# Kernel optimization log

Measured on AMD Instinct MI355X. Metric: run time of the kernel, lower is better.

## Reference

```python
import jax, jax.numpy as jnp
import numpy as np

B, T, D = 4, 2048, 1024
H = 16
DK = D // H


def setup_inputs() -> dict:
    key = jax.random.key(0)
    k1, k2, k3, k4 = jax.random.split(key, 4)
    x = jax.random.normal(k1, (B, T, D), dtype=jnp.float32)
    prefix_lengths = jax.random.randint(k2, (B,), 0, 1024, dtype=jnp.int64)
    # torch Linear weights: [out_features, in_features], scaled like kaiming-uniform-ish
    W_qkv = jax.random.normal(k3, (3 * D, D), dtype=jnp.float32) / np.sqrt(D)
    W_o = jax.random.normal(k4, (D, D), dtype=jnp.float32) / np.sqrt(D)
    return {"x": x, "prefix_lengths": prefix_lengths, "W_qkv": W_qkv, "W_o": W_o}


def _prefix_lm_mask(seq_len, prefix_lengths):
    # True where attention is BLOCKED.
    pos = jnp.arange(seq_len)
    key_pos = pos[None, None, :]          # [1,1,T]
    query_pos = pos[None, :, None]        # [1,T,1]
    prefix = prefix_lengths[:, None, None]  # [B,1,1]
    q_in_pre = query_pos < prefix
    k_in_pre = key_pos < prefix
    block_pre_to_suf = q_in_pre & ~k_in_pre
    block_future_suf = ~q_in_pre & ~k_in_pre & (key_pos > query_pos)
    return block_pre_to_suf | block_future_suf  # [B,T,T]


def reference(x, prefix_lengths, W_qkv, W_o):
    Bb, Tt, Cc = x.shape
    qkv = x @ W_qkv.T                     # [B,T,3D]
    qkv = qkv.reshape(Bb, Tt, 3, H, DK).transpose(2, 0, 3, 1, 4)  # [3,B,H,T,dk]
    q, k, v = qkv[0], qkv[1], qkv[2]
    scale = 1.0 / np.sqrt(DK).astype(np.float32)
    attn = jnp.einsum('bhqd,bhkd->bhqk', q, k) * scale  # [B,H,T,T]
    pl = jnp.clip(prefix_lengths.astype(jnp.int32), 0, Tt)
    mask = _prefix_lm_mask(Tt, pl)        # [B,T,T]
    attn = jnp.where(mask[:, None, :, :], -jnp.inf, attn)
    attn = jax.nn.softmax(attn, axis=-1)
    out = jnp.einsum('bhqk,bhkd->bhqd', attn, v)  # [B,H,T,dk]
    out = out.transpose(0, 2, 1, 3).reshape(Bb, Tt, Cc)
    return out @ W_o.T
```

## Files before the change

### kernel.cpp

```cpp
#include <hip/hip_runtime.h>
#include <stdint.h>

#define NB 4
#define NT 2048
#define ND 1024
#define NH 16
#define NDK 64
#define NTD 3072

typedef __attribute__((ext_vector_type(8))) short short8;
typedef __attribute__((ext_vector_type(4))) float f32x4;
typedef unsigned short u16;
typedef unsigned int u32;

__device__ __forceinline__ u16 f2bf(float f) {
    u32 u = __builtin_bit_cast(u32, f);
    u += 0x7fffu + ((u >> 16) & 1u);
    return (u16)(u >> 16);
}
__device__ __forceinline__ float bf2f(u16 s) {
    u32 u = ((u32)s) << 16;
    return __builtin_bit_cast(float, u);
}

__device__ __forceinline__ void gl_lds16(const u16* g, u16* l) {
    __builtin_amdgcn_global_load_lds(
        (const __attribute__((address_space(1))) u32*)g,
        (__attribute__((address_space(3))) u32*)l, 16, 0, 0);
}

__device__ __forceinline__ int swz(int row, int col) {
    return row * 32 + ((((col >> 3) ^ (row >> 1) ^ (row >> 3)) & 3) << 3) + (col & 7);
}

__global__ __launch_bounds__(256) void cvt_all(const float* __restrict__ x,
                                               const float* __restrict__ wqkv,
                                               const float* __restrict__ wo,
                                               u16* __restrict__ xb,
                                               u16* __restrict__ wqb,
                                               u16* __restrict__ wob) {
    const int n0 = NB * NT * ND;
    const int n1 = 3 * ND * ND;
    int i = (blockIdx.x * 256 + threadIdx.x) * 8;
    const float* src;
    u16* dst;
    if (i < n0) {
        src = x + i; dst = xb + i;
    } else if (i < n0 + n1) {
        src = wqkv + (i - n0); dst = wqb + (i - n0);
    } else {
        src = wo + (i - n0 - n1); dst = wob + (i - n0 - n1);
    }
    float4 a = *(const float4*)(src);
    float4 b = *(const float4*)(src + 4);
    short8 r;
    r[0] = (short)f2bf(a.x); r[1] = (short)f2bf(a.y);
    r[2] = (short)f2bf(a.z); r[3] = (short)f2bf(a.w);
    r[4] = (short)f2bf(b.x); r[5] = (short)f2bf(b.y);
    r[6] = (short)f2bf(b.z); r[7] = (short)f2bf(b.w);
    *(short8*)(dst) = r;
}

template <typename OutT>
__global__ __launch_bounds__(256) void gemm_bt(const u16* __restrict__ A,
                                               const u16* __restrict__ Bm,
                                               OutT* __restrict__ C,
                                               int M, int N, int K) {
    __shared__ __align__(16) u16 As[128 * 32];
    __shared__ __align__(16) u16 Bs[128 * 32];
    const int tid  = threadIdx.x;
    const int wave = tid >> 6, lane = tid & 63;
    const int quad = lane >> 4, l16 = lane & 15;
    const int wm = wave >> 1, wn = wave & 1;
    const int fid = blockIdx.y * gridDim.x + blockIdx.x;
    const int bx = ((fid & 7) << 3) | ((fid >> 3) & 7);
    const int by = fid >> 6;
    const int row0 = bx * 128, col0 = by * 128;

    f32x4 acc[4][4];
#pragma unroll
    for (int i = 0; i < 4; ++i)
#pragma unroll
        for (int j = 0; j < 4; ++j) acc[i][j] = (f32x4){0.f, 0.f, 0.f, 0.f};

    const u16* Ag = A + (size_t)(row0 + (tid >> 2)) * K + ((tid & 3) * 8);
    const u16* Bg = Bm + (size_t)(col0 + (tid >> 2)) * K + ((tid & 3) * 8);
    const size_t stride64 = (size_t)64 * K;
    u16* As0 = As + wave * 512;
    u16* As1 = As + 2048 + wave * 512;
    u16* Bs0 = Bs + wave * 512;
    u16* Bs1 = Bs + 2048 + wave * 512;

    for (int k0 = 0; k0 < K; k0 += 32) {
        gl_lds16(Ag + k0, As0);
        gl_lds16(Ag + k0 + stride64, As1);
        gl_lds16(Bg + k0, Bs0);
        gl_lds16(Bg + k0 + stride64, Bs1);
        __syncthreads();
        short8 af[4], bfr[4];
#pragma unroll
        for (int mi = 0; mi < 4; ++mi)
            af[mi] = *(const short8*)&As[(wm * 64 + mi * 16 + l16) * 32 + quad * 8];
#pragma unroll
        for (int ni = 0; ni < 4; ++ni)
            bfr[ni] = *(const short8*)&Bs[(wn * 64 + ni * 16 + l16) * 32 + quad * 8];
#pragma unroll
        for (int mi = 0; mi < 4; ++mi)
#pragma unroll
            for (int ni = 0; ni < 4; ++ni)
                acc[mi][ni] = __builtin_amdgcn_mfma_f32_16x16x32_bf16(
                    af[mi], bfr[ni], acc[mi][ni], 0, 0, 0);
        __syncthreads();
    }

#pragma unroll
    for (int mi = 0; mi < 4; ++mi) {
#pragma unroll
        for (int ni = 0; ni < 4; ++ni) {
            const int r = row0 + wm * 64 + mi * 16 + quad * 4;
            const int c = col0 + wn * 64 + ni * 16 + l16;
#pragma unroll
            for (int rr = 0; rr < 4; ++rr) {
                float v = acc[mi][ni][rr];
                if constexpr (sizeof(OutT) == 2)
                    C[(size_t)(r + rr) * N + c] = (OutT)f2bf(v);
                else
                    C[(size_t)(r + rr) * N + c] = (OutT)v;
            }
        }
    }
}

__global__ __launch_bounds__(512, 2) void gemm_qk256(const u16* __restrict__ A,
                                                     const u16* __restrict__ Bm,
                                                     u16* __restrict__ Cq) {
    __shared__ __align__(16) u16 rbA[2][8192];
    __shared__ __align__(16) u16 rbB[2][8192];
    u16* const rbAf = &rbA[0][0];
    u16* const rbBf = &rbB[0][0];
    const int tid  = threadIdx.x;
    const int wave = tid >> 6, lane = tid & 63;
    const int quad = lane >> 4, l16 = lane & 15;
    const int wm = wave >> 2, wn = wave & 3;
    const int K = ND;
    const int fid = blockIdx.x;
    const int bx = (fid & 7) * 4 + (fid >> 6);
    const int by = (fid >> 3) & 7;
    const int row0 = bx * 256, col0 = by * 256;

    const int sr0 = tid >> 3, sl0 = (tid & 7) ^ (sr0 & 7);
    const int a1 = 512 + tid;
    const int sr1 = a1 >> 3, sl1 = (a1 & 7) ^ (sr1 & 7);
    const int r0i = 2 * sr0 + (sl0 >> 2), k0i = (sl0 & 3) * 8;
    const int r1i = 2 * sr1 + (sl1 >> 2), k1i = (sl1 & 3) * 8;
    const u16* srcA0 = A + (size_t)(row0 + r0i) * K + k0i;
    const u16* srcA1 = A + (size_t)(row0 + r1i) * K + k1i;
    const u16* srcB0 = Bm + (size_t)(col0 + r0i) * K + k0i;
    const u16* srcB1 = Bm + (size_t)(col0 + r1i) * K + k1i;
    const int ldsc0 = wave * 512;
    const int ldsc1 = 4096 + wave * 512;

    int aoff[8], boff[4];
#pragma unroll
    for (int mi = 0; mi < 8; ++mi) {
        const int row = wm * 128 + mi * 16 + l16;
        const int srow = row >> 1;
        const int slot = ((((row & 1) << 2) | quad) ^ (srow & 7));
        aoff[mi] = srow * 64 + slot * 8;
    }
#pragma unroll
    for (int ni = 0; ni < 4; ++ni) {
        const int row = wn * 64 + ni * 16 + l16;
        const int srow = row >> 1;
        const int slot = ((((row & 1) << 2) | quad) ^ (srow & 7));
        boff[ni] = srow * 64 + slot * 8;
    }

    f32x4 acc[8][4];
#pragma unroll
    for (int i = 0; i < 8; ++i)
#pragma unroll
        for (int j = 0; j < 4; ++j) acc[i][j] = (f32x4){0.f, 0.f, 0.f, 0.f};

    gl_lds16(srcA0, rbAf + ldsc0);
    gl_lds16(srcA1, rbAf + ldsc1);
    gl_lds16(srcB0, rbBf + ldsc0);
    gl_lds16(srcB1, rbBf + ldsc1);
    __syncthreads();

#define QK_TILE(T, TB, NB_)                                                    \
    {                                                                          \
        if ((T) + 1 < 32) {                                                    \
            const int ko = ((T) + 1) * 32;                                     \
            gl_lds16(srcA0 + ko, rbAf + (NB_) + ldsc0);                        \
            gl_lds16(srcA1 + ko, rbAf + (NB_) + ldsc1);                        \
            gl_lds16(srcB0 + ko, rbBf + (NB_) + ldsc0);                        \
            gl_lds16(srcB1 + ko, rbBf + (NB_) + ldsc1);                        \
        }                                                                      \
        short8 af[4], bfr[4];                                                  \
        _Pragma("unroll") for (int mi = 0; mi < 4; ++mi)                       \
            af[mi] = *(const short8*)&rbAf[(TB) + aoff[mi]];                   \
        _Pragma("unroll") for (int ni = 0; ni < 4; ++ni)                       \
            bfr[ni] = *(const short8*)&rbBf[(TB) + boff[ni]];                  \
        __builtin_amdgcn_s_setprio(1);                                         \
        _Pragma("unroll") for (int mi = 0; mi < 4; ++mi)                       \
            _Pragma("unroll") for (int ni = 0; ni < 4; ++ni)                   \
                acc[mi][ni] = __builtin_amdgcn_mfma_f32_16x16x32_bf16(         \
                    af[mi], bfr[ni], acc[mi][ni], 0, 0, 0);                    \
        __builtin_amdgcn_s_setprio(0);                                         \
        __builtin_amdgcn_s_barrier();                                          \
        short8 af2[4];                                                         \
        _Pragma("unroll") for (int mi = 0; mi < 4; ++mi)                       \
            af2[mi] = *(const short8*)&rbAf[(TB) + aoff[4 + mi]];              \
        __builtin_amdgcn_s_setprio(1);                                         \
        _Pragma("unroll") for (int mi = 0; mi < 4; ++mi)                       \
            _Pragma("unroll") for (int ni = 0; ni < 4; ++ni)                   \
                acc[4 + mi][ni] = __builtin_amdgcn_mfma_f32_16x16x32_bf16(     \
                    af2[mi], bfr[ni], acc[4 + mi][ni], 0, 0, 0);               \
        __builtin_amdgcn_s_setprio(0);                                         \
        __syncthreads();                                                       \
    }

    for (int t2 = 0; t2 < 32; t2 += 2) {
        QK_TILE(t2, 0, 8192);
        QK_TILE(t2 + 1, 8192, 0);
    }
#undef QK_TILE

#pragma unroll
    for (int mi = 0; mi < 8; ++mi) {
#pragma unroll
        for (int ni = 0; ni < 4; ++ni) {
            const int r = row0 + wm * 128 + mi * 16 + quad * 4;
            const int c = col0 + wn * 64 + ni * 16 + l16;
#pragma unroll
            for (int rr = 0; rr < 4; ++rr)
                Cq[(size_t)(r + rr) * NTD + c] = f2bf(acc[mi][ni][rr]);
        }
    }
}

__global__ __launch_bounds__(256) void gemm_v(const u16* __restrict__ A,
                                              const u16* __restrict__ Bm,
                                              u16* __restrict__ vtb) {
    const int Kd = ND;
    __shared__ __align__(16) u16 As[128 * 32];
    __shared__ __align__(16) u16 Bs[128 * 32];
    const int tid  = threadIdx.x;
    const int wave = tid >> 6, lane = tid & 63;
    const int quad = lane >> 4, l16 = lane & 15;
    const int wm = wave >> 1, wn = wave & 1;
    const int fid = blockIdx.y * gridDim.x + blockIdx.x;
    const int bx = ((fid & 7) << 3) | ((fid >> 3) & 7);
    const int by = fid >> 6;
    const int row0 = bx * 128, col0 = 2048 + by * 128;

    f32x4 acc[4][4];
#pragma unroll
    for (int i = 0; i < 4; ++i)
#pragma unroll
        for (int j = 0; j < 4; ++j) acc[i][j] = (f32x4){0.f, 0.f, 0.f, 0.f};

    const u16* Ag = A + (size_t)(row0 + (tid >> 2)) * Kd + ((tid & 3) * 8);
    const u16* Bg = Bm + (size_t)(col0 + (tid >> 2)) * Kd + ((tid & 3) * 8);
    const size_t stride64 = (size_t)64 * Kd;
    u16* As0 = As + wave * 512;
    u16* As1 = As + 2048 + wave * 512;
    u16* Bs0 = Bs + wave * 512;
    u16* Bs1 = Bs + 2048 + wave * 512;

    for (int k0 = 0; k0 < Kd; k0 += 32) {
        gl_lds16(Ag + k0, As0);
        gl_lds16(Ag + k0 + stride64, As1);
        gl_lds16(Bg + k0, Bs0);
        gl_lds16(Bg + k0 + stride64, Bs1);
        __syncthreads();
        short8 af[4], bfr[4];
#pragma unroll
        for (int mi = 0; mi < 4; ++mi)
            af[mi] = *(const short8*)&As[(wm * 64 + mi * 16 + l16) * 32 + quad * 8];
#pragma unroll
        for (int ni = 0; ni < 4; ++ni)
            bfr[ni] = *(const short8*)&Bs[(wn * 64 + ni * 16 + l16) * 32 + quad * 8];
#pragma unroll
        for (int mi = 0; mi < 4; ++mi)
#pragma unroll
            for (int ni = 0; ni < 4; ++ni)
                acc[mi][ni] = __builtin_amdgcn_mfma_f32_16x16x32_bf16(
                    af[mi], bfr[ni], acc[mi][ni], 0, 0, 0);
        __syncthreads();
    }

    const int hb = ((col0 - 2048) >> 6) + wn;
    const int bq = (row0 + wm * 64) >> 11;
    const int tb = (row0 + wm * 64) & 2047;
    u16* Ovt = vtb + (size_t)(bq * NH + hb) * 64 * NT + tb;
#pragma unroll
    for (int phase = 0; phase < 2; ++phase) {
        __syncthreads();
        if ((wave >> 1) == phase) {
            u16* L = (wave & 1) ? Bs : As;
#pragma unroll
            for (int mi = 0; mi < 4; ++mi) {
                const int r4 = mi * 4 + quad;
#pragma unroll
                for (int ni = 0; ni < 4; ++ni) {
                    const int cl = ni * 16 + l16;
                    u32 lo = (u32)f2bf(acc[mi][ni][0]) | ((u32)f2bf(acc[mi][ni][1]) << 16);
                    u32 hi = (u32)f2bf(acc[mi][ni][2]) | ((u32)f2bf(acc[mi][ni][3]) << 16);
                    u32* p = (u32*)&L[cl * 64 + (((r4 ^ cl) & 15) << 2)];
                    p[0] = lo; p[1] = hi;
                }
            }
#pragma unroll
            for (int rep = 0; rep < 8; ++rep) {
                const int cl = (lane >> 3) + rep * 8;
                const int tc = lane & 7;
                const u32* p0 = (const u32*)&L[cl * 64 + ((((2 * tc) ^ cl) & 15) << 2)];
                const u32* p1 = (const u32*)&L[cl * 64 + ((((2 * tc + 1) ^ cl) & 15) << 2)];
                u32 o0 = p0[0], o1 = p0[1], o2 = p1[0], o3 = p1[1];
                u32* q = (u32*)(Ovt + (size_t)cl * NT + tc * 8);
                q[0] = o0; q[1] = o1; q[2] = o2; q[3] = o3;
            }
        }
    }
}

#define GETREG_XCC_ID 6164
__global__ __launch_bounds__(256) void flash_prefix(const u16* __restrict__ qkv,
                                                    const u16* __restrict__ vt,
                                                    const int* __restrict__ plen,
                                                    u16* __restrict__ attn,
                                                    u32* __restrict__ ctr) {
    __shared__ __align__(16) u16 Vt2[2][2048];
    __shared__ __align__(16) u16 Kt2[2][2048];
    __shared__ __align__(16) u16 Pl[4 * 512];
    __shared__ int taskS;

    const int tid  = threadIdx.x;
    const int wave = tid >> 6, lane = tid & 63;
    const int quad = lane >> 4, l16 = lane & 15;
    const float QSCALE = 0.18033688f;
    const int ldsoff = wave * 512;

    short8 ones;
#pragma unroll
    for (int j = 0; j < 8; ++j) ones[j] = (short)0x3F80;

    const bool is64 = (plen[1] == 0) && (plen[3] == 0);
    const int xcd = (int)(__builtin_amdgcn_s_getreg(GETREG_XCC_ID) & 7);
    int q = xcd;

    for (;;) {
        if (tid == 0) taskS = (int)atomicAdd(ctr + q * 16, 1u);
        __syncthreads();
        const int pos = taskS;
        if (pos >= 256) {
            q = (q + 1) & 7;
            if (q == xcd) break;
            continue;
        }

        const int bh = (q << 3) | (pos & 7);
        const int b = bh >> 4, h = bh & 15;
        const int q0 = (31 - (pos >> 3)) * 64;

        int P = is64 ? plen[2 * b] : plen[b];
        P = P < 0 ? 0 : (P > NT ? NT : P);

        const u16* Qg = qkv + (size_t)b * NT * NTD + h * NDK;
        const u16* Kg = Qg + ND;
        const u16* Vtb = vt + (size_t)bh * 64 * NT;
        const int qbase = q0 + wave * 16;
        u16* Pw = Pl + wave * 512;

        const int vrow = tid >> 2;
        const int vtq = (tid ^ (vrow >> 1) ^ (vrow >> 3)) & 3;
        const u16* vsrc = Vtb + (size_t)vrow * NT + vtq * 8;
        const int krow = tid >> 3;
        const int kc = (tid ^ krow) & 7;
        const u16* ksrc = Kg + (size_t)krow * NTD + kc * 8;

        short8 qa[2];
#pragma unroll
        for (int kd = 0; kd < 2; ++kd) {
            short8 tq = *(const short8*)(Qg + (size_t)(qbase + l16) * NTD + kd * 32 + quad * 8);
#pragma unroll
            for (int j = 0; j < 8; ++j)
                tq[j] = (short)f2bf(bf2f((u16)tq[j]) * QSCALE);
            qa[kd] = tq;
        }

        f32x4 o[4];
#pragma unroll
        for (int nt = 0; nt < 4; ++nt) o[nt] = (f32x4){0.f, 0.f, 0.f, 0.f};
        f32x4 lsum = (f32x4){0.f, 0.f, 0.f, 0.f};

        int kl[4];
#pragma unroll
        for (int rr = 0; rr < 4; ++rr) {
            const int qrow = qbase + quad * 4 + rr;
            kl[rr] = (qrow < P) ? P : (qrow + 1);
        }
        const int klmin = (qbase < P) ? P : (qbase + 1);
        const int kmax = (q0 + 64 > P) ? (q0 + 64) : P;

        gl_lds16(vsrc, &Vt2[0][ldsoff]);
        gl_lds16(ksrc, &Kt2[0][ldsoff]);
        int buf = 0;

        for (int k0 = 0; k0 < kmax; k0 += 32) {
            __syncthreads();
            if (k0 + 32 < kmax) {
                gl_lds16(vsrc + (k0 + 32), &Vt2[buf ^ 1][ldsoff]);
                gl_lds16(ksrc + (size_t)(k0 + 32) * NTD, &Kt2[buf ^ 1][ldsoff]);
            }
            const u16* Kb = Kt2[buf];
            const u16* Vb = Vt2[buf];

            f32x4 s[2];
#pragma unroll
            for (int ni = 0; ni < 2; ++ni) {
                s[ni] = (f32x4){0.f, 0.f, 0.f, 0.f};
#pragma unroll
                for (int kd = 0; kd < 2; ++kd) {
                    const int r = ni * 16 + l16;
                    const short8 kb = *(const short8*)&Kb[r * 64 + ((((kd * 4 + quad) ^ r) & 7) << 3)];
                    s[ni] = __builtin_amdgcn_mfma_f32_16x16x32_bf16(qa[kd], kb, s[ni], 0, 0, 0);
                }
            }

            const bool full = (k0 + 32 <= klmin);
#pragma unroll
            for (int ni = 0; ni < 2; ++ni) {
#pragma unroll
                for (int rr = 0; rr < 4; ++rr) {
                    float sv = s[ni][rr];
                    if (!full) {
                        const int kpos = k0 + ni * 16 + l16;
                        sv = (kpos < kl[rr]) ? sv : -1e30f;
                    }
                    const float p = exp2f(sv);
                    const u32 u = __builtin_bit_cast(u32, p) + 0x8000u;
                    Pw[swz(quad * 4 + rr, ni * 16 + l16)] = (u16)(u >> 16);
                }
            }

            const short8 pa = *(const short8*)&Pw[swz(l16, quad * 8)];
            lsum = __builtin_amdgcn_mfma_f32_16x16x32_bf16(pa, ones, lsum, 0, 0, 0);
#pragma unroll
            for (int nt = 0; nt < 4; ++nt) {
                const short8 vb = *(const short8*)&Vb[swz(nt * 16 + l16, quad * 8)];
                o[nt] = __builtin_amdgcn_mfma_f32_16x16x32_bf16(pa, vb, o[nt], 0, 0, 0);
            }
            buf ^= 1;
        }

#pragma unroll
        for (int rr = 0; rr < 4; ++rr) {
            const float inv = 1.0f / lsum[rr];
            const size_t rowoff = (size_t)(b * NT + qbase + quad * 4 + rr) * ND + h * NDK;
#pragma unroll
            for (int nt = 0; nt < 4; ++nt)
                attn[rowoff + nt * 16 + l16] = f2bf(o[nt][rr] * inv);
        }
    }
}

extern "C" void kernel_launch(void* const* d_in, const int* in_sizes, int n_in,
                              void* d_out, int out_size, void* d_ws, size_t ws_size,
                              hipStream_t stream) {
    const float* x    = (const float*)d_in[0];
    const int*   plen = (const int*)d_in[1];
    const float* wqkv = (const float*)d_in[2];
    const float* wo   = (const float*)d_in[3];
    float* out = (float*)d_out;

    char* ws = (char*)d_ws;
    u16* xb   = (u16*)(ws);
    u16* wqb  = (u16*)(ws + 16777216);
    u16* wob  = (u16*)(ws + 23068672);
    u16* qkv  = (u16*)(ws + 25165824);
    u16* attn = (u16*)(ws + 75497472);
    u16* vtb  = (u16*)(ws + 92274688);
    u32* ctr  = (u32*)(ws + 75496960);

    hipMemsetAsync(ctr, 0, 512, stream);

    cvt_all<<<6144, 256, 0, stream>>>(x, wqkv, wo, xb, wqb, wob);

    gemm_qk256<<<256, 512, 0, stream>>>(xb, wqb, qkv);

    gemm_v<<<dim3(64, 8), 256, 0, stream>>>(xb, wqb, vtb);

    flash_prefix<<<1024, 256, 0, stream>>>(qkv, vtb, plen, attn, ctr);

    gemm_bt<float><<<dim3(64, 8), 256, 0, stream>>>(attn, wob, out, NB * NT, ND, ND);
}
```

Measured before the change: 292.1 us.

## Deepen QK GEMM LDS pipeline to four stages with vmcnt-based waits

Replaces the double-buffered LDS ring in the QK projection GEMM with a four-buffer ring that keeps three K-tiles of global-to-LDS loads in flight. Explicit s_waitcnt vmcnt counts replace the per-tile __syncthreads, leaving one barrier per iteration, and the mid-tile barrier is dropped. This is meant to hide global load latency and cut synchronisation. In exchange LDS use doubles to 128KB per block, which may limit the two-blocks-per-CU occupancy requested by the launch bounds.

```diff
diff --git a/kernel.cpp b/kernel.cpp
--- a/kernel.cpp
+++ b/kernel.cpp
@@ -134,10 +134,8 @@
 __global__ __launch_bounds__(512, 2) void gemm_qk256(const u16* __restrict__ A,
                                                      const u16* __restrict__ Bm,
                                                      u16* __restrict__ Cq) {
-    __shared__ __align__(16) u16 rbA[2][8192];
-    __shared__ __align__(16) u16 rbB[2][8192];
-    u16* const rbAf = &rbA[0][0];
-    u16* const rbBf = &rbB[0][0];
+    __shared__ __align__(16) u16 rbA[4][8192];
+    __shared__ __align__(16) u16 rbB[4][8192];
     const int tid  = threadIdx.x;
     const int wave = tid >> 6, lane = tid & 63;
     const int quad = lane >> 4, l16 = lane & 15;
@@ -182,50 +180,60 @@
 #pragma unroll
         for (int j = 0; j < 4; ++j) acc[i][j] = (f32x4){0.f, 0.f, 0.f, 0.f};
 
-    gl_lds16(srcA0, rbAf + ldsc0);
-    gl_lds16(srcA1, rbAf + ldsc1);
-    gl_lds16(srcB0, rbBf + ldsc0);
-    gl_lds16(srcB1, rbBf + ldsc1);
-    __syncthreads();
-
-#define QK_TILE(T, TB, NB_)                                                    \
+#define QK_STAGE(T)                                                            \
     {                                                                          \
-        if ((T) + 1 < 32) {                                                    \
-            const int ko = ((T) + 1) * 32;                                     \
-            gl_lds16(srcA0 + ko, rbAf + (NB_) + ldsc0);                        \
-            gl_lds16(srcA1 + ko, rbAf + (NB_) + ldsc1);                        \
-            gl_lds16(srcB0 + ko, rbBf + (NB_) + ldsc0);                        \
-            gl_lds16(srcB1 + ko, rbBf + (NB_) + ldsc1);                        \
-        }                                                                      \
-        short8 af[4], bfr[4];                                                  \
-        _Pragma("unroll") for (int mi = 0; mi < 4; ++mi)                       \
-            af[mi] = *(const short8*)&rbAf[(TB) + aoff[mi]];                   \
-        _Pragma("unroll") for (int ni = 0; ni < 4; ++ni)                       \
-            bfr[ni] = *(const short8*)&rbBf[(TB) + boff[ni]];                  \
-        __builtin_amdgcn_s_setprio(1);                                         \
-        _Pragma("unroll") for (int mi = 0; mi < 4; ++mi)                       \
-            _Pragma("unroll") for (int ni = 0; ni < 4; ++ni)                   \
-                acc[mi][ni] = __builtin_amdgcn_mfma_f32_16x16x32_bf16(         \
-                    af[mi], bfr[ni], acc[mi][ni], 0, 0, 0);                    \
-        __builtin_amdgcn_s_setprio(0);                                         \
-        __builtin_amdgcn_s_barrier();                                          \
-        short8 af2[4];                                                         \
-        _Pragma("unroll") for (int mi = 0; mi < 4; ++mi)                       \
-            af2[mi] = *(const short8*)&rbAf[(TB) + aoff[4 + mi]];              \
-        __builtin_amdgcn_s_setprio(1);                                         \
-        _Pragma("unroll") for (int mi = 0; mi < 4; ++mi)                       \
-            _Pragma("unroll") for (int ni = 0; ni < 4; ++ni)                   \
-                acc[4 + mi][ni] = __builtin_amdgcn_mfma_f32_16x16x32_bf16(     \
-                    af2[mi], bfr[ni], acc[4 + mi][ni], 0, 0, 0);               \
-        __builtin_amdgcn_s_setprio(0);                                         \
-        __syncthreads();                                                       \
-    }
-
-    for (int t2 = 0; t2 < 32; t2 += 2) {
-        QK_TILE(t2, 0, 8192);
-        QK_TILE(t2 + 1, 8192, 0);
-    }
-#undef QK_TILE
+        const int ko_ = (T) * 32;                                              \
+        u16* da_ = &rbA[(T) & 3][0];                                           \
+        u16* db_ = &rbB[(T) & 3][0];                                           \
+        gl_lds16(srcA0 + ko_, da_ + ldsc0);                                    \
+        gl_lds16(srcA1 + ko_, da_ + ldsc1);                                    \
+        gl_lds16(srcB0 + ko_, db_ + ldsc0);                                    \
+        gl_lds16(srcB1 + ko_, db_ + ldsc1);                                    \
+    }
+
+    QK_STAGE(0);
+    QK_STAGE(1);
+    QK_STAGE(2);
+
+    for (int t = 0; t < 32; ++t) {
+        if (t <= 29)      asm volatile("s_waitcnt vmcnt(8)" ::: "memory");
+        else if (t == 30) asm volatile("s_waitcnt vmcnt(4)" ::: "memory");
+        else              asm volatile("s_waitcnt vmcnt(0)" ::: "memory");
+        __builtin_amdgcn_s_barrier();
+        __builtin_amdgcn_sched_barrier(0);
+        if (t + 3 < 32) QK_STAGE(t + 3);
+
+        const u16* At = &rbA[t & 3][0];
+        const u16* Bt = &rbB[t & 3][0];
+        short8 af[4], bfr[4];
+#pragma unroll
+        for (int mi = 0; mi < 4; ++mi)
+            af[mi] = *(const short8*)&At[aoff[mi]];
+#pragma unroll
+        for (int ni = 0; ni < 4; ++ni)
+            bfr[ni] = *(const short8*)&Bt[boff[ni]];
+        __builtin_amdgcn_s_setprio(1);
+#pragma unroll
+        for (int mi = 0; mi < 4; ++mi)
+#pragma unroll
+            for (int ni = 0; ni < 4; ++ni)
+                acc[mi][ni] = __builtin_amdgcn_mfma_f32_16x16x32_bf16(
+                    af[mi], bfr[ni], acc[mi][ni], 0, 0, 0);
+        __builtin_amdgcn_s_setprio(0);
+        short8 af2[4];
+#pragma unroll
+        for (int mi = 0; mi < 4; ++mi)
+            af2[mi] = *(const short8*)&At[aoff[4 + mi]];
+        __builtin_amdgcn_s_setprio(1);
+#pragma unroll
+        for (int mi = 0; mi < 4; ++mi)
+#pragma unroll
+            for (int ni = 0; ni < 4; ++ni)
+                acc[4 + mi][ni] = __builtin_amdgcn_mfma_f32_16x16x32_bf16(
+                    af2[mi], bfr[ni], acc[4 + mi][ni], 0, 0, 0);
+        __builtin_amdgcn_s_setprio(0);
+    }
+#undef QK_STAGE
 
 #pragma unroll
     for (int mi = 0; mi < 8; ++mi) {
```

New measurement: 298.1 us. +2.1%, slower.

## Process 64-key tiles per barrier and raise wave priority around MFMA blocks

Applied to the files above, without the earlier changes.

The flash attention loop now stages two 32-key K/V sub-tiles per double-buffer slot, so each iteration covers 64 keys and needs half as many __syncthreads barriers and prefetch rounds. It also wraps the MFMA groups in s_setprio to favour matrix issue across waves. This doubles the K/V LDS footprint, which may reduce occupancy. It also adds a partial-tile skip for the second half, and that skip assumes kmax is a multiple of 32.

```diff
diff --git a/kernel.cpp b/kernel.cpp
--- a/kernel.cpp
+++ b/kernel.cpp
@@ -332,8 +332,8 @@
                                                     const int* __restrict__ plen,
                                                     u16* __restrict__ attn,
                                                     u32* __restrict__ ctr) {
-    __shared__ __align__(16) u16 Vt2[2][2048];
-    __shared__ __align__(16) u16 Kt2[2][2048];
+    __shared__ __align__(16) u16 Vt2[2][2][2048];
+    __shared__ __align__(16) u16 Kt2[2][2][2048];
     __shared__ __align__(16) u16 Pl[4 * 512];
     __shared__ int taskS;
 
@@ -405,53 +405,67 @@
         const int klmin = (qbase < P) ? P : (qbase + 1);
         const int kmax = (q0 + 64 > P) ? (q0 + 64) : P;
 
-        gl_lds16(vsrc, &Vt2[0][ldsoff]);
-        gl_lds16(ksrc, &Kt2[0][ldsoff]);
+        gl_lds16(vsrc, &Vt2[0][0][ldsoff]);
+        gl_lds16(vsrc + 32, &Vt2[0][1][ldsoff]);
+        gl_lds16(ksrc, &Kt2[0][0][ldsoff]);
+        gl_lds16(ksrc + (size_t)32 * NTD, &Kt2[0][1][ldsoff]);
         int buf = 0;
 
-        for (int k0 = 0; k0 < kmax; k0 += 32) {
+        for (int k0 = 0; k0 < kmax; k0 += 64) {
             __syncthreads();
-            if (k0 + 32 < kmax) {
-                gl_lds16(vsrc + (k0 + 32), &Vt2[buf ^ 1][ldsoff]);
-                gl_lds16(ksrc + (size_t)(k0 + 32) * NTD, &Kt2[buf ^ 1][ldsoff]);
+            if (k0 + 64 < kmax) {
+                gl_lds16(vsrc + (k0 + 64), &Vt2[buf ^ 1][0][ldsoff]);
+                gl_lds16(vsrc + (k0 + 96), &Vt2[buf ^ 1][1][ldsoff]);
+                gl_lds16(ksrc + (size_t)(k0 + 64) * NTD, &Kt2[buf ^ 1][0][ldsoff]);
+                gl_lds16(ksrc + (size_t)(k0 + 96) * NTD, &Kt2[buf ^ 1][1][ldsoff]);
             }
-            const u16* Kb = Kt2[buf];
-            const u16* Vb = Vt2[buf];
-
-            f32x4 s[2];
-#pragma unroll
-            for (int ni = 0; ni < 2; ++ni) {
-                s[ni] = (f32x4){0.f, 0.f, 0.f, 0.f};
-#pragma unroll
-                for (int kd = 0; kd < 2; ++kd) {
-                    const int r = ni * 16 + l16;
-                    const short8 kb = *(const short8*)&Kb[r * 64 + ((((kd * 4 + quad) ^ r) & 7) << 3)];
-                    s[ni] = __builtin_amdgcn_mfma_f32_16x16x32_bf16(qa[kd], kb, s[ni], 0, 0, 0);
+
+#pragma unroll
+            for (int hh = 0; hh < 2; ++hh) {
+                const int kh = k0 + 32 * hh;
+                if (hh == 1 && kh >= kmax) continue;
+                const u16* Kb = Kt2[buf][hh];
+                const u16* Vb = Vt2[buf][hh];
+
+                f32x4 s[2];
+                __builtin_amdgcn_s_setprio(1);
+#pragma unroll
+                for (int ni = 0; ni < 2; ++ni) {
+                    s[ni] = (f32x4){0.f, 0.f, 0.f, 0.f};
+#pragma unroll
+                    for (int kd = 0; kd < 2; ++kd) {
+                        const int r = ni * 16 + l16;
+                        const short8 kb = *(const short8*)&Kb[r * 64 + ((((kd * 4 + quad) ^ r) & 7) << 3)];
+                        s[ni] = __builtin_amdgcn_mfma_f32_16x16x32_bf16(qa[kd], kb, s[ni], 0, 0, 0);
+                    }
                 }
-            }
-
-            const bool full = (k0 + 32 <= klmin);
-#pragma unroll
-            for (int ni = 0; ni < 2; ++ni) {
-#pragma unroll
-                for (int rr = 0; rr < 4; ++rr) {
-                    float sv = s[ni][rr];
-                    if (!full) {
-                        const int kpos = k0 + ni * 16 + l16;
-                        sv = (kpos < kl[rr]) ? sv : -1e30f;
+                __builtin_amdgcn_s_setprio(0);
+
+                const bool full = (kh + 32 <= klmin);
+#pragma unroll
+                for (int ni = 0; ni < 2; ++ni) {
+#pragma unroll
+                    for (int rr = 0; rr < 4; ++rr) {
+                        float sv = s[ni][rr];
+                        if (!full) {
+                            const int kpos = kh + ni * 16 + l16;
+                            sv = (kpos < kl[rr]) ? sv : -1e30f;
+                        }
+                        const float p = exp2f(sv);
+                        const u32 u = __builtin_bit_cast(u32, p) + 0x8000u;
+                        Pw[swz(quad * 4 + rr, ni * 16 + l16)] = (u16)(u >> 16);
                     }
-                    const float p = exp2f(sv);
-                    const u32 u = __builtin_bit_cast(u32, p) + 0x8000u;
-                    Pw[swz(quad * 4 + rr, ni * 16 + l16)] = (u16)(u >> 16);
                 }
-            }
-
-            const short8 pa = *(const short8*)&Pw[swz(l16, quad * 8)];
-            lsum = __builtin_amdgcn_mfma_f32_16x16x32_bf16(pa, ones, lsum, 0, 0, 0);
-#pragma unroll
-            for (int nt = 0; nt < 4; ++nt) {
-                const short8 vb = *(const short8*)&Vb[swz(nt * 16 + l16, quad * 8)];
-                o[nt] = __builtin_amdgcn_mfma_f32_16x16x32_bf16(pa, vb, o[nt], 0, 0, 0);
+
+                const short8 pa = *(const short8*)&Pw[swz(l16, quad * 8)];
+                __builtin_amdgcn_s_setprio(1);
+                lsum = __builtin_amdgcn_mfma_f32_16x16x32_bf16(pa, ones, lsum, 0, 0, 0);
+#pragma unroll
+                for (int nt = 0; nt < 4; ++nt) {
+                    const short8 vb = *(const short8*)&Vb[swz(nt * 16 + l16, quad * 8)];
+                    o[nt] = __builtin_amdgcn_mfma_f32_16x16x32_bf16(pa, vb, o[nt], 0, 0, 0);
+                }
+                __builtin_amdgcn_s_setprio(0);
             }
             buf ^= 1;
         }
```

Result: no change. 297.3 us (+1.8%).

## Replace output projection GEMM with 256x128 double-buffered swizzled-LDS kernel

Applied to the files above, without the earlier changes.

Swaps the generic 128x128 single-buffered output-projection GEMM for a dedicated 256x128-tile kernel with 512 threads, double-buffered LDS, XOR-swizzled LDS layout and prefetch of the next K tile while MFMAs run. It follows the design already used by the QK projection kernel. The aim is to hide global-load latency, reduce LDS bank conflicts and halve the block count. In exchange it uses more registers and LDS per block and a split-barrier scheme that must stay correct.

```diff
diff --git a/kernel.cpp b/kernel.cpp
--- a/kernel.cpp
+++ b/kernel.cpp
@@ -61,72 +61,109 @@
     *(short8*)(dst) = r;
 }
 
-template <typename OutT>
-__global__ __launch_bounds__(256) void gemm_bt(const u16* __restrict__ A,
-                                               const u16* __restrict__ Bm,
-                                               OutT* __restrict__ C,
-                                               int M, int N, int K) {
-    __shared__ __align__(16) u16 As[128 * 32];
-    __shared__ __align__(16) u16 Bs[128 * 32];
+__global__ __launch_bounds__(512, 2) void gemm_bt256(const u16* __restrict__ A,
+                                                     const u16* __restrict__ Bm,
+                                                     float* __restrict__ C) {
+    __shared__ __align__(16) u16 rbA[2][8192];
+    __shared__ __align__(16) u16 rbB[2][4096];
+    u16* const rbAf = &rbA[0][0];
+    u16* const rbBf = &rbB[0][0];
     const int tid  = threadIdx.x;
     const int wave = tid >> 6, lane = tid & 63;
     const int quad = lane >> 4, l16 = lane & 15;
-    const int wm = wave >> 1, wn = wave & 1;
-    const int fid = blockIdx.y * gridDim.x + blockIdx.x;
-    const int bx = ((fid & 7) << 3) | ((fid >> 3) & 7);
-    const int by = fid >> 6;
-    const int row0 = bx * 128, col0 = by * 128;
-
-    f32x4 acc[4][4];
-#pragma unroll
-    for (int i = 0; i < 4; ++i)
-#pragma unroll
-        for (int j = 0; j < 4; ++j) acc[i][j] = (f32x4){0.f, 0.f, 0.f, 0.f};
-
-    const u16* Ag = A + (size_t)(row0 + (tid >> 2)) * K + ((tid & 3) * 8);
-    const u16* Bg = Bm + (size_t)(col0 + (tid >> 2)) * K + ((tid & 3) * 8);
-    const size_t stride64 = (size_t)64 * K;
-    u16* As0 = As + wave * 512;
-    u16* As1 = As + 2048 + wave * 512;
-    u16* Bs0 = Bs + wave * 512;
-    u16* Bs1 = Bs + 2048 + wave * 512;
-
-    for (int k0 = 0; k0 < K; k0 += 32) {
-        gl_lds16(Ag + k0, As0);
-        gl_lds16(Ag + k0 + stride64, As1);
-        gl_lds16(Bg + k0, Bs0);
-        gl_lds16(Bg + k0 + stride64, Bs1);
-        __syncthreads();
-        short8 af[4], bfr[4];
-#pragma unroll
-        for (int mi = 0; mi < 4; ++mi)
-            af[mi] = *(const short8*)&As[(wm * 64 + mi * 16 + l16) * 32 + quad * 8];
-#pragma unroll
-        for (int ni = 0; ni < 4; ++ni)
-            bfr[ni] = *(const short8*)&Bs[(wn * 64 + ni * 16 + l16) * 32 + quad * 8];
-#pragma unroll
-        for (int mi = 0; mi < 4; ++mi)
-#pragma unroll
-            for (int ni = 0; ni < 4; ++ni)
-                acc[mi][ni] = __builtin_amdgcn_mfma_f32_16x16x32_bf16(
-                    af[mi], bfr[ni], acc[mi][ni], 0, 0, 0);
-        __syncthreads();
-    }
-
-#pragma unroll
-    for (int mi = 0; mi < 4; ++mi) {
-#pragma unroll
-        for (int ni = 0; ni < 4; ++ni) {
-            const int r = row0 + wm * 64 + mi * 16 + quad * 4;
-            const int c = col0 + wn * 64 + ni * 16 + l16;
-#pragma unroll
-            for (int rr = 0; rr < 4; ++rr) {
-                float v = acc[mi][ni][rr];
-                if constexpr (sizeof(OutT) == 2)
-                    C[(size_t)(r + rr) * N + c] = (OutT)f2bf(v);
-                else
-                    C[(size_t)(r + rr) * N + c] = (OutT)v;
-            }
+    const int wm = wave >> 2, wn = wave & 3;
+    const int K = ND;
+    const int fid = blockIdx.x;
+    const int bx = (fid & 7) * 4 + (fid >> 6);
+    const int by = (fid >> 3) & 7;
+    const int row0 = bx * 256, col0 = by * 128;
+
+    const int sr0 = tid >> 3, sl0 = (tid & 7) ^ (sr0 & 7);
+    const int a1 = 512 + tid;
+    const int sr1 = a1 >> 3, sl1 = (a1 & 7) ^ (sr1 & 7);
+    const int r0i = 2 * sr0 + (sl0 >> 2), k0i = (sl0 & 3) * 8;
+    const int r1i = 2 * sr1 + (sl1 >> 2), k1i = (sl1 & 3) * 8;
+    const u16* srcA0 = A + (size_t)(row0 + r0i) * K + k0i;
+    const u16* srcA1 = A + (size_t)(row0 + r1i) * K + k1i;
+    const u16* srcB0 = Bm + (size_t)(col0 + r0i) * K + k0i;
+    const int ldscA0 = wave * 512;
+    const int ldscA1 = 4096 + wave * 512;
+    const int ldscB0 = wave * 512;
+
+    int aoff[8], boff[2];
+#pragma unroll
+    for (int mi = 0; mi < 8; ++mi) {
+        const int row = wm * 128 + mi * 16 + l16;
+        const int srow = row >> 1;
+        const int slot = ((((row & 1) << 2) | quad) ^ (srow & 7));
+        aoff[mi] = srow * 64 + slot * 8;
+    }
+#pragma unroll
+    for (int ni = 0; ni < 2; ++ni) {
+        const int row = wn * 32 + ni * 16 + l16;
+        const int srow = row >> 1;
+        const int slot = ((((row & 1) << 2) | quad) ^ (srow & 7));
+        boff[ni] = srow * 64 + slot * 8;
+    }
+
+    f32x4 acc[8][2];
+#pragma unroll
+    for (int i = 0; i < 8; ++i)
+#pragma unroll
+        for (int j = 0; j < 2; ++j) acc[i][j] = (f32x4){0.f, 0.f, 0.f, 0.f};
+
+    gl_lds16(srcA0, rbAf + ldscA0);
+    gl_lds16(srcA1, rbAf + ldscA1);
+    gl_lds16(srcB0, rbBf + ldscB0);
+    __syncthreads();
+
+#define BT_TILE(T, AB, BB, NAB, NBB)                                           \
+    {                                                                          \
+        if ((T) + 1 < 32) {                                                    \
+            const int ko = ((T) + 1) * 32;                                     \
+            gl_lds16(srcA0 + ko, rbAf + (NAB) + ldscA0);                       \
+            gl_lds16(srcA1 + ko, rbAf + (NAB) + ldscA1);                       \
+            gl_lds16(srcB0 + ko, rbBf + (NBB) + ldscB0);                       \
+        }                                                                      \
+        short8 af[4], bfr[2];                                                  \
+        _Pragma("unroll") for (int mi = 0; mi < 4; ++mi)                       \
+            af[mi] = *(const short8*)&rbAf[(AB) + aoff[mi]];                   \
+        _Pragma("unroll") for (int ni = 0; ni < 2; ++ni)                       \
+            bfr[ni] = *(const short8*)&rbBf[(BB) + boff[ni]];                  \
+        __builtin_amdgcn_s_setprio(1);                                         \
+        _Pragma("unroll") for (int mi = 0; mi < 4; ++mi)                       \
+            _Pragma("unroll") for (int ni = 0; ni < 2; ++ni)                   \
+                acc[mi][ni] = __builtin_amdgcn_mfma_f32_16x16x32_bf16(         \
+                    af[mi], bfr[ni], acc[mi][ni], 0, 0, 0);                    \
+        __builtin_amdgcn_s_setprio(0);                                         \
+        __builtin_amdgcn_s_barrier();                                          \
+        short8 af2[4];                                                         \
+        _Pragma("unroll") for (int mi = 0; mi < 4; ++mi)                       \
+            af2[mi] = *(const short8*)&rbAf[(AB) + aoff[4 + mi]];              \
+        __builtin_amdgcn_s_setprio(1);                                         \
+        _Pragma("unroll") for (int mi = 0; mi < 4; ++mi)                       \
+            _Pragma("unroll") for (int ni = 0; ni < 2; ++ni)                   \
+                acc[4 + mi][ni] = __builtin_amdgcn_mfma_f32_16x16x32_bf16(     \
+                    af2[mi], bfr[ni], acc[4 + mi][ni], 0, 0, 0);               \
+        __builtin_amdgcn_s_setprio(0);                                         \
+        __syncthreads();                                                       \
+    }
+
+    for (int t2 = 0; t2 < 32; t2 += 2) {
+        BT_TILE(t2, 0, 0, 8192, 4096);
+        BT_TILE(t2 + 1, 8192, 4096, 0, 0);
+    }
+#undef BT_TILE
+
+#pragma unroll
+    for (int mi = 0; mi < 8; ++mi) {
+#pragma unroll
+        for (int ni = 0; ni < 2; ++ni) {
+            const int r = row0 + wm * 128 + mi * 16 + quad * 4;
+            const int c = col0 + wn * 32 + ni * 16 + l16;
+#pragma unroll
+            for (int rr = 0; rr < 4; ++rr)
+                C[(size_t)(r + rr) * ND + c] = acc[mi][ni][rr];
         }
     }
 }
@@ -495,5 +532,5 @@
 
     flash_prefix<<<1024, 256, 0, stream>>>(qkv, vtb, plen, attn, ctr);
 
-    gemm_bt<float><<<dim3(64, 8), 256, 0, stream>>>(attn, wob, out, NB * NT, ND, ND);
-}
+    gemm_bt256<<<256, 512, 0, stream>>>(attn, wob, out);
+}
```

After: 295.8 us. Within noise of the previous version (+1.3%).
